# Optimization experiments

Measured on AMD Instinct MI355X. Metric: run time of the kernel, lower is better.

Reference implementation:

```python
import jax, jax.numpy as jnp
import numpy as np

IMG = 1024.0
NMS_THRESH = 0.7
PRE_NMS_TOPK = 1000
POST_NMS_TOPK = 1000
MIN_BOX_SIZE = 0.0
SCALE_CLAMP = float(np.log(1000.0 / 16.0))
NEG = -1e9
LVL_OFFSET = 2.0 * IMG  # batched_nms coordinate-offset trick: boxes from different levels never overlap

_STRIDES = [4, 8, 16, 32, 64]
_SIZES = [32.0, 64.0, 128.0, 256.0, 512.0]
_RATIOS = [0.5, 1.0, 2.0]


def _make_anchors():
    """Detectron2 DefaultAnchorGenerator anchors (offset=0)."""
    out = []
    for s, size in zip(_STRIDES, _SIZES):
        area = size * size
        base = []
        for r in _RATIOS:
            w = np.sqrt(area / r)
            h = r * w
            base.append([-w / 2.0, -h / 2.0, w / 2.0, h / 2.0])
        base = np.asarray(base, np.float32)  # [A,4]
        H = int(IMG) // s
        coords = np.arange(H, dtype=np.float32) * s
        sx, sy = np.meshgrid(coords, coords)
        shifts = np.stack([sx.ravel(), sy.ravel(), sx.ravel(), sy.ravel()], axis=1)  # [HW,4]
        anchors = (shifts[:, None, :] + base[None, :, :]).reshape(-1, 4).astype(np.float32)
        out.append(jnp.asarray(anchors))
    return out


def setup_inputs() -> dict:
    key = jax.random.key(0)
    N = 4
    names = ["p2", "p3", "p4", "p5", "p6"]
    anchors = _make_anchors()
    inp = {}
    for i, (nm, an) in enumerate(zip(names, anchors)):
        HWA = an.shape[0]
        k1 = jax.random.fold_in(key, 2 * i)
        k2 = jax.random.fold_in(key, 2 * i + 1)
        inp[f"logits_{nm}"] = jax.random.normal(k1, (N, HWA), jnp.float32)
        # small deltas so decoded proposals stay realistic
        inp[f"deltas_{nm}"] = 0.1 * jax.random.normal(k2, (N, HWA, 4), jnp.float32)
        inp[f"anchors_{nm}"] = an
    return inp


def _apply_deltas(deltas, anchors):
    """Box2BoxTransform.apply_deltas with weights (1,1,1,1)."""
    wa = anchors[..., 2] - anchors[..., 0]
    ha = anchors[..., 3] - anchors[..., 1]
    cxa = anchors[..., 0] + 0.5 * wa
    cya = anchors[..., 1] + 0.5 * ha
    dx, dy, dw, dh = (deltas[..., i] for i in range(4))
    dw = jnp.minimum(dw, SCALE_CLAMP)
    dh = jnp.minimum(dh, SCALE_CLAMP)
    cx = dx * wa + cxa
    cy = dy * ha + cya
    w = wa * jnp.exp(dw)
    h = ha * jnp.exp(dh)
    return jnp.stack([cx - 0.5 * w, cy - 0.5 * h, cx + 0.5 * w, cy + 0.5 * h], axis=-1)


def _pairwise_iou(b):
    area = (b[:, 2] - b[:, 0]) * (b[:, 3] - b[:, 1])
    lt = jnp.maximum(b[:, None, :2], b[None, :, :2])
    rb = jnp.minimum(b[:, None, 2:], b[None, :, 2:])
    wh = jnp.clip(rb - lt, 0.0)
    inter = wh[..., 0] * wh[..., 1]
    return inter / (area[:, None] + area[None, :] - inter + 1e-9)


def _nms_single(boxes, scores, lvl):
    """Greedy batched NMS (per-level via coordinate offset) + post-NMS top-k. boxes [M,4]."""
    M = boxes.shape[0]
    order = jnp.argsort(-scores)
    boxes = boxes[order]
    scores = scores[order]
    lvl = lvl[order]
    off_boxes = boxes + (lvl.astype(boxes.dtype) * LVL_OFFSET)[:, None]
    iou = _pairwise_iou(off_boxes)  # [M,M]
    valid = scores > NEG / 2
    idx = jnp.arange(M)

    def body(supp, xs):
        row, i, v = xs
        keep_i = (~supp[i]) & v
        supp = supp | (keep_i & (row > NMS_THRESH) & (idx > i))
        return supp, None

    supp, _ = jax.lax.scan(body, jnp.zeros((M,), bool), (iou, idx, valid))
    kept_scores = jnp.where((~supp) & valid, scores, NEG)
    top_s, top_i = jax.lax.top_k(kept_scores, POST_NMS_TOPK)
    return boxes[top_i], top_s


def _forward(logits_list, deltas_list, anchors_list):
    all_b, all_s, all_l = [], [], []
    for li, (lg, dl, an) in enumerate(zip(logits_list, deltas_list, anchors_list)):
        props = _apply_deltas(dl, an[None, :, :])  # [N,HWA,4]
        k = min(PRE_NMS_TOPK, lg.shape[1])
        sc, idx = jax.lax.top_k(lg, k)  # per-level pre-NMS top-k
        bx = jnp.take_along_axis(props, idx[..., None], axis=1)
        all_b.append(bx)
        all_s.append(sc)
        all_l.append(jnp.full((k,), li, jnp.int32))
    boxes = jnp.concatenate(all_b, axis=1)  # [N,M,4]
    scores = jnp.concatenate(all_s, axis=1)  # [N,M]
    lvl = jnp.concatenate(all_l, axis=0)  # [M]
    # clip to image + min-size filter (min_box_size = 0)
    boxes = jnp.clip(boxes, 0.0, IMG)
    w = boxes[..., 2] - boxes[..., 0]
    h = boxes[..., 3] - boxes[..., 1]
    scores = jnp.where((w > MIN_BOX_SIZE) & (h > MIN_BOX_SIZE), scores, NEG)
    return jax.vmap(_nms_single, in_axes=(0, 0, None))(boxes, scores, lvl)


def reference(logits_p2, logits_p3, logits_p4, logits_p5, logits_p6,
              deltas_p2, deltas_p3, deltas_p4, deltas_p5, deltas_p6,
              anchors_p2, anchors_p3, anchors_p4, anchors_p5, anchors_p6):
    logits = [logits_p2, logits_p3, logits_p4, logits_p5, logits_p6]
    deltas = [deltas_p2, deltas_p3, deltas_p4, deltas_p5, deltas_p6]
    anchors = [anchors_p2, anchors_p3, anchors_p4, anchors_p5, anchors_p6]
    boxes, scores = _forward(logits, deltas, anchors)
    return boxes, scores
```

## Files before the change

kernel.cpp:

```cpp
#include <hip/hip_runtime.h>
#include <stdint.h>
#include <math.h>

#define NLVL 5
#define NIMG 4
#define NGRP (NIMG * NLVL)
#define M_TOT 4768
#define POST_K 1000
#define NEGV  (-1e9f)
#define CAP 2048
#define BPI 65
#define TRI_W 7680
#define RD_SPLIT 8
#define UCAP 2048

__constant__ int c_hwa[NLVL]  = {196608, 49152, 12288, 3072, 768};
__constant__ int c_k[NLVL]    = {1000, 1000, 1000, 1000, 768};
__constant__ int c_base[NLVL] = {0, 1000, 2000, 3000, 4000};
__constant__ int c_cnt[NLVL]  = {4096, 4096, 4096, 3072, 768};
__constant__ int c_us[NLVL]   = {0, 48, 60, 63, 64};
__constant__ int c_un[NLVL]   = {48, 12, 3, 1, 1};
__constant__ uint32_t c_T0[NLVL] = {0xC019999Au, 0xBFECCCCDu, 0xBF933333u, 0x80000000u, 0x00000000u};

struct Ptrs {
    const float* logits[NLVL];
    const float* deltas[NLVL];
    const float* anchors[NLVL];
};

__device__ __forceinline__ uint32_t flipf(float f) {
    uint32_t b = __float_as_uint(f);
    return (b & 0x80000000u) ? ~b : (b | 0x80000000u);
}
__device__ __forceinline__ float unflipf(uint32_t key) {
    uint32_t b = (key & 0x80000000u) ? (key & 0x7FFFFFFFu) : ~key;
    return __uint_as_float(b);
}
__device__ __forceinline__ float rdlane_f(float v, int l) {
    return __uint_as_float((uint32_t)__builtin_amdgcn_readlane((int)__float_as_uint(v), l));
}

__device__ __forceinline__ void grp_decompose(int g, int& img, int& lvl, int& off, int& cnt) {
    img = g / BPI;
    int r = g % BPI;
    if (r < 48)      { lvl = 0; off = r * 4096; }
    else if (r < 60) { lvl = 1; off = (r - 48) * 4096; }
    else if (r < 63) { lvl = 2; off = (r - 60) * 4096; }
    else if (r < 64) { lvl = 3; off = 0; }
    else             { lvl = 4; off = 0; }
    cnt = c_cnt[lvl];
}

__device__ __forceinline__ uint32_t wave_or32(uint32_t v) {
    v |= (uint32_t)__builtin_amdgcn_update_dpp(0, (int)v, 0x111, 0xf, 0xf, true);
    v |= (uint32_t)__builtin_amdgcn_update_dpp(0, (int)v, 0x112, 0xf, 0xf, true);
    v |= (uint32_t)__builtin_amdgcn_update_dpp(0, (int)v, 0x114, 0xf, 0xf, true);
    v |= (uint32_t)__builtin_amdgcn_update_dpp(0, (int)v, 0x118, 0xf, 0xf, true);
    v |= (uint32_t)__builtin_amdgcn_update_dpp(0, (int)v, 0x142, 0xf, 0xf, true);
    v |= (uint32_t)__builtin_amdgcn_update_dpp(0, (int)v, 0x143, 0xf, 0xf, true);
    return (uint32_t)__builtin_amdgcn_readlane((int)v, 63);
}

__global__ void kCompactSpec(Ptrs p, uint32_t* __restrict__ ucnt,
                             uint64_t* __restrict__ pk2) {
    int img, lvl, off, cnt;
    const int u = blockIdx.x;
    grp_decompose(u, img, lvl, off, cnt);
    const int tid = threadIdx.x;
    const float* lg = p.logits[lvl] + (size_t)img * c_hwa[lvl] + off;
    const uint32_t T = c_T0[lvl];

    __shared__ uint32_t scnt;
    __shared__ uint64_t sbuf[4096];
    if (tid == 0) scnt = 0u;
    __syncthreads();

    const int nvec = cnt >> 2;
    const float4* lg4 = (const float4*)lg;
    for (int v = tid; v < nvec; v += 256) {
        float4 x = lg4[v];
        float xs[4] = {x.x, x.y, x.z, x.w};
        #pragma unroll
        for (int c = 0; c < 4; ++c) {
            uint32_t key = flipf(xs[c]);
            if (key >= T) {
                uint32_t pos = atomicAdd(&scnt, 1u);
                uint32_t eidx = (uint32_t)(off + 4 * v + c);
                sbuf[pos] = ((uint64_t)key << 32) | (uint32_t)(~eidx);
            }
        }
    }
    __syncthreads();
    const uint32_t n = scnt;
    if (tid == 0) ucnt[u] = n;
    const uint32_t nw = min(n, (uint32_t)UCAP);
    uint64_t* pk = pk2 + (size_t)u * UCAP;
    for (uint32_t i = tid; i < nw; i += 256) pk[i] = sbuf[i];
}

__global__ void kRankDecode(Ptrs p, const uint32_t* __restrict__ ucnt,
                            const uint64_t* __restrict__ pk2,
                            float* __restrict__ cand_box,
                            float* __restrict__ cand_score) {
    #pragma clang fp contract(off)
    const int blk = blockIdx.x;
    const int grp = blk / RD_SPLIT;
    const int sub = blk % RD_SPLIT;
    const int img = grp / NLVL;
    const int lvl = grp % NLVL;
    const int n    = c_hwa[lvl];
    const int k    = c_k[lvl];
    const int base = c_base[lvl];
    const int tid = threadIdx.x;
    const int nu  = c_un[lvl];
    const int u0  = img * BPI + c_us[lvl];
    const int c0  = sub * (CAP / RD_SPLIT);

    __shared__ uint64_t K[CAP];
    __shared__ int soff[49];
    __shared__ uint32_t hist[256];
    __shared__ uint32_t sh_pre, sh_rem, scnt2;
    __shared__ int scc, sbad;

    if (tid == 0) {
        int o = 0, bad = 0;
        for (int i = 0; i < nu; ++i) {
            int c = (int)ucnt[u0 + i];
            soff[i] = o;
            if (c > UCAP) bad = 1;
            o += c;
        }
        soff[nu] = o;
        scc = o; sbad = bad;
    }
    __syncthreads();
    int cc = scc;
    const bool fb = sbad || (cc < k) || (cc > CAP);

    if (!fb) {
        if (c0 >= cc) return;
        uint64_t vb[8];
        int tt[8];
        #pragma unroll
        for (int q = 0; q < 8; ++q) {
            const int t = tid + q * 256;
            tt[q] = t;
            if (t < cc) {
                int lo2 = 0, hi2 = nu - 1;
                while (lo2 < hi2) {
                    int mid = (lo2 + hi2 + 1) >> 1;
                    if (soff[mid] <= t) lo2 = mid; else hi2 = mid - 1;
                }
                vb[q] = pk2[(size_t)(u0 + lo2) * UCAP + (t - soff[lo2])];
            }
        }
        #pragma unroll
        for (int q = 0; q < 8; ++q)
            if (tt[q] < cc) K[tt[q]] = vb[q];
        __syncthreads();
    } else {
        const float* lg = p.logits[lvl] + (size_t)img * n;
        if (tid == 0) { sh_pre = 0u; sh_rem = (uint32_t)k; scnt2 = 0u; }
        for (int pass = 0; pass < 4; ++pass) {
            hist[tid] = 0u;
            __syncthreads();
            const int shift = 24 - 8 * pass;
            const uint32_t pre = sh_pre;
            for (int i = tid; i < n; i += 256) {
                uint32_t key = flipf(lg[i]);
                if (pass == 0 || (key >> (shift + 8)) == pre)
                    atomicAdd(&hist[(key >> shift) & 255u], 1u);
            }
            __syncthreads();
            if (tid == 0) {
                uint32_t rem = sh_rem;
                int d = 255;
                for (; d > 0; --d) {
                    uint32_t c = hist[d];
                    if (rem <= c) break;
                    rem -= c;
                }
                sh_rem = rem;
                sh_pre = (pre << 8) | (uint32_t)d;
            }
            __syncthreads();
        }
        const uint32_t T = sh_pre;
        for (int i = tid; i < n; i += 256) {
            uint32_t key = flipf(lg[i]);
            if (key >= T) {
                uint32_t pos = atomicAdd(&scnt2, 1u);
                if (pos < CAP) K[pos] = ((uint64_t)key << 32) | (uint32_t)(~(uint32_t)i);
            }
        }
        __syncthreads();
        cc = (int)min(scnt2, (uint32_t)CAP);
        if (c0 >= cc) return;
    }

    const int c = c0 + tid;
    const uint64_t myK = (c < cc) ? K[c] : ~0ull;
    int r = 0;
    int j = 0;
    for (; j + 8 <= cc; j += 8) {
        #pragma unroll
        for (int u = 0; u < 8; ++u) r += (int)(K[j + u] > myK);
    }
    for (; j < cc; ++j) r += (int)(K[j] > myK);

    if (c >= cc || r >= k) return;

    uint32_t key = (uint32_t)(myK >> 32);
    uint32_t ic  = ~(uint32_t)(myK & 0xFFFFFFFFu);
    const float* an = p.anchors[lvl] + (size_t)ic * 4;
    const float* dl = p.deltas[lvl] + ((size_t)img * n + ic) * 4;
    float a0 = an[0], a1 = an[1], a2 = an[2], a3 = an[3];
    float wa = a2 - a0, ha = a3 - a1;
    float cxa = a0 + 0.5f * wa, cya = a1 + 0.5f * ha;
    float dx = dl[0], dy = dl[1], dw = dl[2], dh = dl[3];
    const float SC = (float)4.135166556742356;
    dw = fminf(dw, SC);
    dh = fminf(dh, SC);
    float cx = dx * wa + cxa, cy = dy * ha + cya;
    float w = wa * expf(dw), h = ha * expf(dh);
    float x1 = cx - 0.5f * w, y1 = cy - 0.5f * h;
    float x2 = cx + 0.5f * w, y2 = cy + 0.5f * h;
    x1 = fminf(fmaxf(x1, 0.0f), 1024.0f);
    y1 = fminf(fmaxf(y1, 0.0f), 1024.0f);
    x2 = fminf(fmaxf(x2, 0.0f), 1024.0f);
    y2 = fminf(fmaxf(y2, 0.0f), 1024.0f);
    float bw = x2 - x1, bh = y2 - y1;
    float score = (bw > 0.0f && bh > 0.0f) ? unflipf(key) : NEGV;
    const int slot = base + r;
    float* ob = cand_box + ((size_t)img * M_TOT + slot) * 4;
    ob[0] = x1; ob[1] = y1; ob[2] = x2; ob[3] = y2;
    cand_score[(size_t)img * M_TOT + slot] = score;
}

__global__ void kIou(const float* __restrict__ cand_box,
                     uint64_t* __restrict__ tri, uint64_t* __restrict__ diag) {
    #pragma clang fp contract(off)
    const int blk = blockIdx.x;
    const int grp = blk >> 6;
    const int w   = (blk >> 2) & 15;
    const int ch  = blk & 3;
    const int img = grp / NLVL;
    const int lvl = grp % NLVL;
    const int k    = c_k[lvl];
    const int base = c_base[lvl];
    if (64 * w >= k) return;
    const int R  = min(64 * (w + 1), k);
    const int r0 = ch * 256;
    if (r0 >= R) return;
    const int jn = min(64, k - 64 * w);
    const float lo = (float)lvl * 2048.0f;
    const int tid = threadIdx.x;
    const int lane = tid & 63;

    const int jl = (lane < jn) ? lane : 0;
    const float4 jb = *(const float4*)(cand_box + ((size_t)img * M_TOT + base + 64 * w + jl) * 4);
    const float jx1r = jb.x + lo, jy1r = jb.y + lo;
    const float jx2r = jb.z + lo, jy2r = jb.w + lo;
    const float jarr = (jx2r - jx1r) * (jy2r - jy1r);

    const int r = r0 + tid;
    const bool act = r < R;
    float rx1 = 0, ry1 = 0, rx2 = 0, ry2 = 0, ra = 0;
    if (act) {
        const float4 b = *(const float4*)(cand_box + ((size_t)img * M_TOT + base + r) * 4);
        rx1 = b.x + lo; ry1 = b.y + lo; rx2 = b.z + lo; ry2 = b.w + lo;
        ra = (rx2 - rx1) * (ry2 - ry1);
    }

    uint64_t bits = 0ull;
    #pragma unroll 4
    for (int jj = 0; jj < jn; ++jj) {
        const float bx1 = rdlane_f(jx1r, jj);
        const float by1 = rdlane_f(jy1r, jj);
        const float bx2 = rdlane_f(jx2r, jj);
        const float by2 = rdlane_f(jy2r, jj);
        const float bar = rdlane_f(jarr, jj);
        const int j = 64 * w + jj;
        if (j > r) {
            float ltx = fmaxf(rx1, bx1);
            float lty = fmaxf(ry1, by1);
            float rbx = fminf(rx2, bx2);
            float rby = fminf(ry2, by2);
            float wx = fmaxf(rbx - ltx, 0.0f);
            float wy = fmaxf(rby - lty, 0.0f);
            float inter = wx * wy;
            float denom = ((ra + bar) - inter) + 1e-9f;
            if (inter / denom > 0.7f) bits |= (1ull << jj);
        }
    }

    if (act) {
        if ((r >> 6) == w) diag[(size_t)grp * 1024 + r] = bits;
        else               tri[(size_t)grp * TRI_W + 32 * w * (w - 1) + r] = bits;
    }
}

__global__ void kScan(const float* __restrict__ cand_score,
                      const uint64_t* __restrict__ tri,
                      const uint64_t* __restrict__ diag,
                      uint32_t* __restrict__ kept) {
    const int grp = blockIdx.x;
    const int img = grp / NLVL;
    const int lvl = grp % NLVL;
    const int k    = c_k[lvl];
    const int base = c_base[lvl];
    const int lane = threadIdx.x;

    __shared__ uint64_t sdiag[1024];
    __shared__ uint64_t sinv[16];

    const uint64_t* dg_g = diag + (size_t)grp * 1024;
    #pragma unroll
    for (int s = 0; s < 16; ++s) {
        const int r = 64 * s + lane;
        uint64_t d = (r < k) ? dg_g[r] : 0ull;
        sdiag[r] = d;
        float sc = (r < k) ? cand_score[(size_t)img * M_TOT + base + r] : NEGV;
        uint64_t iv = __ballot(sc <= -5e8f);
        if (lane == 0) sinv[s] = iv;
    }
    __syncthreads();

    const uint64_t* trig = tri + (size_t)grp * TRI_W;
    uint32_t mykept = 0u;
    const int nstage = (k + 63) >> 6;

    #pragma unroll 1
    for (int q = 0; q < nstage; ++q) {
        const uint64_t* tq = trig + 32 * q * (q - 1);
        uint64_t vals[15];
        #pragma unroll
        for (int s = 0; s < 15; ++s)
            if (s < q) vals[s] = tq[64 * s + lane];
        uint64_t v = 0ull;
        #pragma unroll
        for (int s = 0; s < 15; ++s)
            if (s < q) {
                uint64_t msk = (uint64_t)0 - (uint64_t)((mykept >> s) & 1u);
                v |= vals[s] & msk;
            }
        const uint32_t vlo = wave_or32((uint32_t)v);
        const uint32_t vhi = wave_or32((uint32_t)(v >> 32));
        const uint64_t invq = sinv[q];
        const uint32_t ivlo = __builtin_amdgcn_readfirstlane((uint32_t)invq);
        const uint32_t ivhi = __builtin_amdgcn_readfirstlane((uint32_t)(invq >> 32));
        uint64_t rem = ~((((uint64_t)ivhi << 32) | (uint64_t)ivlo)
                       | (((uint64_t)vhi  << 32) | (uint64_t)vlo));

        const uint64_t darrq = sdiag[64 * q + lane];
        const uint32_t dlo = (uint32_t)darrq, dhi = (uint32_t)(darrq >> 32);
        const uint64_t nz = __ballot(darrq != 0ull);

        uint64_t kw = 0ull;
        for (;;) {
            uint64_t t = rem & nz;
            if (t == 0ull) { kw |= rem; break; }
            const int m = (int)__builtin_ctzll(t);
            const uint64_t bm = 1ull << m;
            const uint64_t lowm = bm - 1ull;
            kw |= (rem & lowm) | bm;
            const uint64_t dg =
                ((uint64_t)(uint32_t)__builtin_amdgcn_readlane((int)dhi, m) << 32)
              |  (uint64_t)(uint32_t)__builtin_amdgcn_readlane((int)dlo, m);
            rem &= ~(lowm | bm | dg);
        }
        mykept |= ((uint32_t)((kw >> lane) & 1ull)) << q;
    }

    #pragma unroll
    for (int s = 0; s < 16; ++s) {
        const int r = 64 * s + lane;
        if (r < k)
            kept[(size_t)img * M_TOT + base + r] = (mykept >> s) & 1u;
    }
}

__device__ __forceinline__ int bs_count_ge(const uint32_t* a, int n, uint32_t x) {
    int lo = 0, hi = n;
    while (lo < hi) { int mid = (lo + hi) >> 1; if (a[mid] >= x) lo = mid + 1; else hi = mid; }
    return lo;
}
__device__ __forceinline__ int bs_count_gt(const uint32_t* a, int n, uint32_t x) {
    int lo = 0, hi = n;
    while (lo < hi) { int mid = (lo + hi) >> 1; if (a[mid] > x) lo = mid + 1; else hi = mid; }
    return lo;
}

__global__ void kMergeOut(const float* __restrict__ cand_box,
                          const float* __restrict__ cand_score,
                          const uint32_t* __restrict__ kept,
                          float* __restrict__ out) {
    const int img = blockIdx.x;
    const int tid = threadIdx.x;
    const int lane = tid & 63, wave = tid >> 6;

    __shared__ uint32_t vkey[NLVL * 1024];
    __shared__ uint32_t ord[M_TOT];
    __shared__ uint32_t wsum[NLVL][16];
    __shared__ int wtot[16];

    uint32_t mykey[NLVL];
    int myvalid[NLVL], mylower[NLVL];
    #pragma unroll
    for (int L = 0; L < NLVL; ++L) {
        const int kL = c_k[L];
        const bool act = tid < kL;
        float s = act ? cand_score[(size_t)img * M_TOT + c_base[L] + tid] : NEGV;
        bool valid = act && (s > -5e8f);
        uint64_t mask = __ballot(valid);
        mylower[L] = (int)__popcll(mask & ((1ull << lane) - 1ull));
        if (lane == 0) wsum[L][wave] = (uint32_t)__popcll(mask);
        mykey[L] = flipf(s);
        myvalid[L] = valid ? 1 : 0;
    }
    __syncthreads();

    int nv[NLVL], myvpre[NLVL];
    #pragma unroll
    for (int L = 0; L < NLVL; ++L) {
        int pw = 0, tot = 0;
        #pragma unroll
        for (int w = 0; w < 16; ++w) {
            if (w < wave) pw += (int)wsum[L][w];
            tot += (int)wsum[L][w];
        }
        nv[L] = tot;
        myvpre[L] = pw + mylower[L];
        if (tid < c_k[L] && myvalid[L])
            vkey[L * 1024 + myvpre[L]] = mykey[L];
    }
    int totalValid = 0;
    #pragma unroll
    for (int L = 0; L < NLVL; ++L) totalValid += nv[L];
    __syncthreads();

    int invBase = totalValid;
    #pragma unroll
    for (int L = 0; L < NLVL; ++L) {
        const int kL = c_k[L];
        if (tid < kL) {
            const int slot = c_base[L] + tid;
            if (myvalid[L]) {
                const uint32_t x = mykey[L];
                int pos = myvpre[L];
                #pragma unroll
                for (int Lp = 0; Lp < NLVL; ++Lp) {
                    if (Lp == L) continue;
                    pos += (Lp < L) ? bs_count_ge(&vkey[Lp * 1024], nv[Lp], x)
                                    : bs_count_gt(&vkey[Lp * 1024], nv[Lp], x);
                }
                const uint32_t kp = kept[(size_t)img * M_TOT + slot];
                ord[pos] = (uint32_t)slot | (kp << 31);
            } else {
                const int inv_idx = tid - myvpre[L];
                ord[invBase + inv_idx] = (uint32_t)slot;
            }
        }
        invBase += (c_k[L] - nv[L]);
    }
    __syncthreads();

    const int PT = 5;
    const int pos0 = tid * PT;
    int flags[PT];
    uint32_t slots[PT];
    int lsum = 0;
    #pragma unroll
    for (int q = 0; q < PT; ++q) {
        int pp = pos0 + q;
        int kf = 0; uint32_t sl = 0;
        if (pp < M_TOT) {
            uint32_t o = ord[pp];
            sl = o & 0x7FFFFFFFu;
            kf = (int)(o >> 31);
        }
        flags[q] = kf; slots[q] = sl; lsum += kf;
    }
    int incl = lsum;
    #pragma unroll
    for (int off = 1; off < 64; off <<= 1) {
        int t = __shfl_up(incl, off, 64);
        if (lane >= off) incl += t;
    }
    if (lane == 63) wtot[wave] = incl;
    __syncthreads();
    int wpre = 0, total = 0;
    #pragma unroll
    for (int w = 0; w < 16; ++w) {
        int v = wtot[w];
        if (w < wave) wpre += v;
        total += v;
    }
    const int excl = wpre + (incl - lsum);

    int run = 0;
    #pragma unroll
    for (int q = 0; q < PT; ++q) {
        int pp = pos0 + q;
        if (pp >= M_TOT) break;
        int kf = flags[q];
        int kbefore = excl + run;
        run += kf;
        int oidx = kf ? kbefore : (total + (pp - kbefore));
        if (oidx < POST_K) {
            uint32_t sl = slots[q];
            const float4 b = *(const float4*)(cand_box + ((size_t)img * M_TOT + sl) * 4);
            float* ob = out + ((size_t)img * POST_K + oidx) * 4;
            ob[0] = b.x; ob[1] = b.y; ob[2] = b.z; ob[3] = b.w;
            out[NIMG * POST_K * 4 + (size_t)img * POST_K + oidx] =
                kf ? cand_score[(size_t)img * M_TOT + sl] : NEGV;
        }
    }
}

extern "C" void kernel_launch(void* const* d_in, const int* in_sizes, int n_in,
                              void* d_out, int out_size, void* d_ws, size_t ws_size,
                              hipStream_t stream) {
    Ptrs p;
    for (int l = 0; l < NLVL; ++l) {
        p.logits[l]  = (const float*)d_in[3 * l + 0];
        p.deltas[l]  = (const float*)d_in[3 * l + 1];
        p.anchors[l] = (const float*)d_in[3 * l + 2];
    }

    char* w = (char*)d_ws;
    float* cand_box   = (float*)w;        w += (size_t)NIMG * M_TOT * 4 * sizeof(float);
    float* cand_score = (float*)w;        w += (size_t)NIMG * M_TOT * sizeof(float);
    uint32_t* kept        = (uint32_t*)w; w += (size_t)NIMG * M_TOT * sizeof(uint32_t);
    uint64_t* pk2         = (uint64_t*)w; w += (size_t)NIMG * BPI * UCAP * sizeof(uint64_t);
    uint64_t* tri         = (uint64_t*)w; w += (size_t)NGRP * TRI_W * sizeof(uint64_t);
    uint64_t* diag        = (uint64_t*)w; w += (size_t)NGRP * 1024 * sizeof(uint64_t);
    uint32_t* ucnt        = (uint32_t*)w; w += (size_t)NIMG * BPI * sizeof(uint32_t);

    kCompactSpec<<<NIMG * BPI,       256, 0, stream>>>(p, ucnt, pk2);
    kRankDecode <<<NGRP * RD_SPLIT,  256, 0, stream>>>(p, ucnt, pk2, cand_box, cand_score);
    kIou        <<<NGRP * 64,        256, 0, stream>>>(cand_box, tri, diag);
    kScan       <<<NGRP,              64, 0, stream>>>(cand_score, tri, diag, kept);
    kMergeOut   <<<NIMG,            1024, 0, stream>>>(cand_box, cand_score, kept, (float*)d_out);
}
```

Baseline: 185.4 us.

## Fuse NMS scan into merge kernel and split compaction into smaller chunks

The per-level greedy NMS scan kernel is merged into the per-image merge/output kernel. Five waves of a 1024-thread block each scan one level, and the kept flags stay in shared memory, which removes one launch and the global kept buffer round-trip. Separately, the compaction stage now uses 2048-element chunks (128 blocks per image instead of 65) for more parallelism, and the rank/decode kernel stages per-chunk counts through shared memory. The trade-off is that the scan now runs on only 4 blocks, with the other waves idle during it, and the decode stage must merge more chunks.

Measured after the change: 209.5 us. +13.0%, slower.

```diff
diff --git a/kernel.cpp b/kernel.cpp
--- a/kernel.cpp
+++ b/kernel.cpp
@@ -9,7 +9,7 @@
 #define POST_K 1000
 #define NEGV  (-1e9f)
 #define CAP 2048
-#define BPI 65
+#define BPI 128
 #define TRI_W 7680
 #define RD_SPLIT 8
 #define UCAP 2048
@@ -17,9 +17,9 @@
 __constant__ int c_hwa[NLVL]  = {196608, 49152, 12288, 3072, 768};
 __constant__ int c_k[NLVL]    = {1000, 1000, 1000, 1000, 768};
 __constant__ int c_base[NLVL] = {0, 1000, 2000, 3000, 4000};
-__constant__ int c_cnt[NLVL]  = {4096, 4096, 4096, 3072, 768};
-__constant__ int c_us[NLVL]   = {0, 48, 60, 63, 64};
-__constant__ int c_un[NLVL]   = {48, 12, 3, 1, 1};
+__constant__ int c_cnt[NLVL]  = {2048, 2048, 2048, 3072, 768};
+__constant__ int c_us[NLVL]   = {0, 96, 120, 126, 127};
+__constant__ int c_un[NLVL]   = {96, 24, 6, 1, 1};
 __constant__ uint32_t c_T0[NLVL] = {0xC019999Au, 0xBFECCCCDu, 0xBF933333u, 0x80000000u, 0x00000000u};
 
 struct Ptrs {
@@ -43,11 +43,11 @@
 __device__ __forceinline__ void grp_decompose(int g, int& img, int& lvl, int& off, int& cnt) {
     img = g / BPI;
     int r = g % BPI;
-    if (r < 48)      { lvl = 0; off = r * 4096; }
-    else if (r < 60) { lvl = 1; off = (r - 48) * 4096; }
-    else if (r < 63) { lvl = 2; off = (r - 60) * 4096; }
-    else if (r < 64) { lvl = 3; off = 0; }
-    else             { lvl = 4; off = 0; }
+    if (r < 96)       { lvl = 0; off = r * 2048; }
+    else if (r < 120) { lvl = 1; off = (r - 96) * 2048; }
+    else if (r < 126) { lvl = 2; off = (r - 120) * 2048; }
+    else if (r < 127) { lvl = 3; off = 0; }
+    else              { lvl = 4; off = 0; }
     cnt = c_cnt[lvl];
 }
 
@@ -71,7 +71,7 @@
     const uint32_t T = c_T0[lvl];
 
     __shared__ uint32_t scnt;
-    __shared__ uint64_t sbuf[4096];
+    __shared__ uint64_t sbuf[3072];
     if (tid == 0) scnt = 0u;
     __syncthreads();
 
@@ -117,15 +117,18 @@
     const int c0  = sub * (CAP / RD_SPLIT);
 
     __shared__ uint64_t K[CAP];
-    __shared__ int soff[49];
+    __shared__ uint32_t sucnt[96];
+    __shared__ int soff[97];
     __shared__ uint32_t hist[256];
     __shared__ uint32_t sh_pre, sh_rem, scnt2;
     __shared__ int scc, sbad;
 
+    if (tid < nu) sucnt[tid] = ucnt[u0 + tid];
+    __syncthreads();
     if (tid == 0) {
         int o = 0, bad = 0;
         for (int i = 0; i < nu; ++i) {
-            int c = (int)ucnt[u0 + i];
+            int c = (int)sucnt[i];
             soff[i] = o;
             if (c > UCAP) bad = 1;
             o += c;
@@ -300,86 +303,6 @@
     }
 }
 
-__global__ void kScan(const float* __restrict__ cand_score,
-                      const uint64_t* __restrict__ tri,
-                      const uint64_t* __restrict__ diag,
-                      uint32_t* __restrict__ kept) {
-    const int grp = blockIdx.x;
-    const int img = grp / NLVL;
-    const int lvl = grp % NLVL;
-    const int k    = c_k[lvl];
-    const int base = c_base[lvl];
-    const int lane = threadIdx.x;
-
-    __shared__ uint64_t sdiag[1024];
-    __shared__ uint64_t sinv[16];
-
-    const uint64_t* dg_g = diag + (size_t)grp * 1024;
-    #pragma unroll
-    for (int s = 0; s < 16; ++s) {
-        const int r = 64 * s + lane;
-        uint64_t d = (r < k) ? dg_g[r] : 0ull;
-        sdiag[r] = d;
-        float sc = (r < k) ? cand_score[(size_t)img * M_TOT + base + r] : NEGV;
-        uint64_t iv = __ballot(sc <= -5e8f);
-        if (lane == 0) sinv[s] = iv;
-    }
-    __syncthreads();
-
-    const uint64_t* trig = tri + (size_t)grp * TRI_W;
-    uint32_t mykept = 0u;
-    const int nstage = (k + 63) >> 6;
-
-    #pragma unroll 1
-    for (int q = 0; q < nstage; ++q) {
-        const uint64_t* tq = trig + 32 * q * (q - 1);
-        uint64_t vals[15];
-        #pragma unroll
-        for (int s = 0; s < 15; ++s)
-            if (s < q) vals[s] = tq[64 * s + lane];
-        uint64_t v = 0ull;
-        #pragma unroll
-        for (int s = 0; s < 15; ++s)
-            if (s < q) {
-                uint64_t msk = (uint64_t)0 - (uint64_t)((mykept >> s) & 1u);
-                v |= vals[s] & msk;
-            }
-        const uint32_t vlo = wave_or32((uint32_t)v);
-        const uint32_t vhi = wave_or32((uint32_t)(v >> 32));
-        const uint64_t invq = sinv[q];
-        const uint32_t ivlo = __builtin_amdgcn_readfirstlane((uint32_t)invq);
-        const uint32_t ivhi = __builtin_amdgcn_readfirstlane((uint32_t)(invq >> 32));
-        uint64_t rem = ~((((uint64_t)ivhi << 32) | (uint64_t)ivlo)
-                       | (((uint64_t)vhi  << 32) | (uint64_t)vlo));
-
-        const uint64_t darrq = sdiag[64 * q + lane];
-        const uint32_t dlo = (uint32_t)darrq, dhi = (uint32_t)(darrq >> 32);
-        const uint64_t nz = __ballot(darrq != 0ull);
-
-        uint64_t kw = 0ull;
-        for (;;) {
-            uint64_t t = rem & nz;
-            if (t == 0ull) { kw |= rem; break; }
-            const int m = (int)__builtin_ctzll(t);
-            const uint64_t bm = 1ull << m;
-            const uint64_t lowm = bm - 1ull;
-            kw |= (rem & lowm) | bm;
-            const uint64_t dg =
-                ((uint64_t)(uint32_t)__builtin_amdgcn_readlane((int)dhi, m) << 32)
-              |  (uint64_t)(uint32_t)__builtin_amdgcn_readlane((int)dlo, m);
-            rem &= ~(lowm | bm | dg);
-        }
-        mykept |= ((uint32_t)((kw >> lane) & 1ull)) << q;
-    }
-
-    #pragma unroll
-    for (int s = 0; s < 16; ++s) {
-        const int r = 64 * s + lane;
-        if (r < k)
-            kept[(size_t)img * M_TOT + base + r] = (mykept >> s) & 1u;
-    }
-}
-
 __device__ __forceinline__ int bs_count_ge(const uint32_t* a, int n, uint32_t x) {
     int lo = 0, hi = n;
     while (lo < hi) { int mid = (lo + hi) >> 1; if (a[mid] >= x) lo = mid + 1; else hi = mid; }
@@ -391,18 +314,95 @@
     return lo;
 }
 
-__global__ void kMergeOut(const float* __restrict__ cand_box,
-                          const float* __restrict__ cand_score,
-                          const uint32_t* __restrict__ kept,
-                          float* __restrict__ out) {
+__global__ void kScanMerge(const float* __restrict__ cand_box,
+                           const float* __restrict__ cand_score,
+                           const uint64_t* __restrict__ tri,
+                           const uint64_t* __restrict__ diag,
+                           float* __restrict__ out) {
     const int img = blockIdx.x;
     const int tid = threadIdx.x;
     const int lane = tid & 63, wave = tid >> 6;
 
-    __shared__ uint32_t vkey[NLVL * 1024];
-    __shared__ uint32_t ord[M_TOT];
+    __shared__ __align__(16) char uA[40960];
+    __shared__ uint32_t skept[M_TOT];
+    __shared__ uint64_t sinv5[NLVL][16];
     __shared__ uint32_t wsum[NLVL][16];
     __shared__ int wtot[16];
+
+    if (wave < NLVL) {
+        const int lvl = wave;
+        const int grp = img * NLVL + lvl;
+        const int k    = c_k[lvl];
+        const int base = c_base[lvl];
+        uint64_t* sdiag = ((uint64_t*)uA) + lvl * 1024;
+
+        const uint64_t* dg_g = diag + (size_t)grp * 1024;
+        #pragma unroll
+        for (int s = 0; s < 16; ++s) {
+            const int r = 64 * s + lane;
+            uint64_t d = (r < k) ? dg_g[r] : 0ull;
+            sdiag[r] = d;
+            float sc = (r < k) ? cand_score[(size_t)img * M_TOT + base + r] : NEGV;
+            uint64_t iv = __ballot(sc <= -5e8f);
+            if (lane == 0) sinv5[lvl][s] = iv;
+        }
+
+        const uint64_t* trig = tri + (size_t)grp * TRI_W;
+        uint32_t mykept = 0u;
+        const int nstage = (k + 63) >> 6;
+
+        #pragma unroll 1
+        for (int q = 0; q < nstage; ++q) {
+            const uint64_t* tq = trig + 32 * q * (q - 1);
+            uint64_t vals[15];
+            #pragma unroll
+            for (int s = 0; s < 15; ++s)
+                if (s < q) vals[s] = tq[64 * s + lane];
+            uint64_t v = 0ull;
+            #pragma unroll
+            for (int s = 0; s < 15; ++s)
+                if (s < q) {
+                    uint64_t msk = (uint64_t)0 - (uint64_t)((mykept >> s) & 1u);
+                    v |= vals[s] & msk;
+                }
+            const uint32_t vlo = wave_or32((uint32_t)v);
+            const uint32_t vhi = wave_or32((uint32_t)(v >> 32));
+            const uint64_t invq = sinv5[lvl][q];
+            const uint32_t ivlo = __builtin_amdgcn_readfirstlane((uint32_t)invq);
+            const uint32_t ivhi = __builtin_amdgcn_readfirstlane((uint32_t)(invq >> 32));
+            uint64_t rem = ~((((uint64_t)ivhi << 32) | (uint64_t)ivlo)
+                           | (((uint64_t)vhi  << 32) | (uint64_t)vlo));
+
+            const uint64_t darrq = sdiag[64 * q + lane];
+            const uint32_t dlo = (uint32_t)darrq, dhi = (uint32_t)(darrq >> 32);
+            const uint64_t nz = __ballot(darrq != 0ull);
+
+            uint64_t kw = 0ull;
+            for (;;) {
+                uint64_t t = rem & nz;
+                if (t == 0ull) { kw |= rem; break; }
+                const int m = (int)__builtin_ctzll(t);
+                const uint64_t bm = 1ull << m;
+                const uint64_t lowm = bm - 1ull;
+                kw |= (rem & lowm) | bm;
+                const uint64_t dg =
+                    ((uint64_t)(uint32_t)__builtin_amdgcn_readlane((int)dhi, m) << 32)
+                  |  (uint64_t)(uint32_t)__builtin_amdgcn_readlane((int)dlo, m);
+                rem &= ~(lowm | bm | dg);
+            }
+            mykept |= ((uint32_t)((kw >> lane) & 1ull)) << q;
+        }
+
+        #pragma unroll
+        for (int s = 0; s < 16; ++s) {
+            const int r = 64 * s + lane;
+            if (r < k) skept[base + r] = (mykept >> s) & 1u;
+        }
+    }
+    __syncthreads();
+
+    uint32_t* vkey = (uint32_t*)uA;
+    uint32_t* ord  = ((uint32_t*)uA) + 5120;
 
     uint32_t mykey[NLVL];
     int myvalid[NLVL], mylower[NLVL];
@@ -454,14 +454,13 @@
                     pos += (Lp < L) ? bs_count_ge(&vkey[Lp * 1024], nv[Lp], x)
                                     : bs_count_gt(&vkey[Lp * 1024], nv[Lp], x);
                 }
-                const uint32_t kp = kept[(size_t)img * M_TOT + slot];
-                ord[pos] = (uint32_t)slot | (kp << 31);
+                ord[pos] = (uint32_t)slot | (skept[slot] << 31);
             } else {
                 const int inv_idx = tid - myvpre[L];
                 ord[invBase + inv_idx] = (uint32_t)slot;
             }
         }
-        invBase += (c_k[L] - nv[L]);
+        invBase += (kL - nv[L]);
     }
     __syncthreads();
 
@@ -531,7 +530,6 @@
     char* w = (char*)d_ws;
     float* cand_box   = (float*)w;        w += (size_t)NIMG * M_TOT * 4 * sizeof(float);
     float* cand_score = (float*)w;        w += (size_t)NIMG * M_TOT * sizeof(float);
-    uint32_t* kept        = (uint32_t*)w; w += (size_t)NIMG * M_TOT * sizeof(uint32_t);
     uint64_t* pk2         = (uint64_t*)w; w += (size_t)NIMG * BPI * UCAP * sizeof(uint64_t);
     uint64_t* tri         = (uint64_t*)w; w += (size_t)NGRP * TRI_W * sizeof(uint64_t);
     uint64_t* diag        = (uint64_t*)w; w += (size_t)NGRP * 1024 * sizeof(uint64_t);
@@ -540,6 +538,6 @@
     kCompactSpec<<<NIMG * BPI,       256, 0, stream>>>(p, ucnt, pk2);
     kRankDecode <<<NGRP * RD_SPLIT,  256, 0, stream>>>(p, ucnt, pk2, cand_box, cand_score);
     kIou        <<<NGRP * 64,        256, 0, stream>>>(cand_box, tri, diag);
-    kScan       <<<NGRP,              64, 0, stream>>>(cand_score, tri, diag, kept);
-    kMergeOut   <<<NIMG,            1024, 0, stream>>>(cand_box, cand_score, kept, (float*)d_out);
-}
+    kScanMerge  <<<NIMG,            1024, 0, stream>>>(cand_box, cand_score, tri, diag,
+                                                       (float*)d_out);
+}
```
